# Performance work log

Measured on AMD Instinct MI355X. Metric: run time of the kernel, lower is better.

Reference implementation:

```python
import jax, jax.numpy as jnp
import numpy as np
from jax import lax

N, C, A, H, W = 32, 512, 256, 64, 64

def _maxpool2(t):
    # 2x2 max pool, stride 2, NCHW
    return lax.reduce_window(t, -jnp.inf, lax.max, (1, 1, 2, 2), (1, 1, 2, 2), 'VALID')

def setup_inputs() -> dict:
    key = jax.random.key(0)
    ks = jax.random.split(key, 5)
    return {
        'x': jax.random.normal(ks[0], (N, C, H, W), dtype=jnp.float32),
        'w_g': jax.random.normal(ks[1], (A, C), dtype=jnp.float32) * 0.02,
        'b_g': jax.random.normal(ks[2], (A,), dtype=jnp.float32) * 0.02,
        'w_phi': jax.random.normal(ks[3], (A, C), dtype=jnp.float32) * 0.02,
        'b_phi': jax.random.normal(ks[4], (A,), dtype=jnp.float32) * 0.02,
    }

def reference(x, w_g, b_g, w_phi, b_phi):
    n, c, h, w = x.shape
    # g: 1x1 conv in->attn, flattened spatial: (N, A, H*W)
    g_x = (jnp.einsum('nchw,ac->nahw', x, w_g) + b_g[None, :, None, None]).reshape(n, A, h * w)
    # theta: maxpool of x, (N, C, HW/4)
    theta_x = _maxpool2(x).reshape(n, c, -1)
    # phi: 1x1 conv then maxpool, (N, HW/4, A)
    phi_conv = jnp.einsum('nchw,ac->nahw', x, w_phi) + b_phi[None, :, None, None]
    phi_x = _maxpool2(phi_conv).reshape(n, A, -1)  # (N, A, HW/4)
    # channel-attention scores: (N, C, A)
    cmat = jnp.einsum('ncm,nam->nca', theta_x, phi_x)
    attn = jax.nn.softmax(cmat, axis=-1)
    # aggregate: (N, C, HW)
    y = jnp.einsum('nca,nal->ncl', attn, g_x)
    z = y.reshape(n, c, h, w)
    return z + x
```

## Files before the change

### kernel.cpp

```cpp
#include <hip/hip_runtime.h>


typedef _Float16 half8 __attribute__((ext_vector_type(8)));
typedef _Float16 half4v __attribute__((ext_vector_type(4)));
typedef float f32x4 __attribute__((ext_vector_type(4)));

#define NB 32
#define CD 512
#define AD 256
#define PD 4096
#define PPD 1024

#define OFF_XT    0UL
#define OFF_WC    134217728UL
#define OFF_THETA 134742016UL
#define OFF_GT    168296448UL
#define OFF_PHI   235405312UL
#define OFF_ATTN  252182528UL

#define GLOAD16(gp, lp) \
    __builtin_amdgcn_global_load_lds((const __attribute__((address_space(1))) void*)(gp), \
                                     (__attribute__((address_space(3))) void*)(lp), 16, 0, 0)

__device__ __forceinline__ int swz_off(int row, int q) {
    return row * 32 + ((q ^ ((row >> 1) & 3)) * 8);
}

template <int LD>
__device__ __forceinline__ void stage2(const _Float16* __restrict__ Ab,
                                       const _Float16* __restrict__ Bb,
                                       int k0, _Float16* bufA, _Float16* bufB, int t) {
#pragma unroll
    for (int j = 0; j < 4; ++j) {
        int idx = j * 256 + t;
        int ci = idx & 511;
        int row = ci >> 2, chP = ci & 3;
        int chL = chP ^ ((row >> 1) & 3);
        const _Float16* src = ((idx < 512) ? Ab : Bb) + (size_t)row * LD + k0 + chL * 8;
        _Float16* dst = ((idx < 512) ? bufA : bufB) + ci * 8;
        GLOAD16(src, dst);
    }
}

__global__ __launch_bounds__(256) void k_prep_w(const float* __restrict__ w_g,
                                                const float* __restrict__ w_phi,
                                                _Float16* __restrict__ Wc) {
    int idx4 = blockIdx.x * 256 + threadIdx.x;
    int flat = idx4 * 4;
    const float* src = (flat < AD * CD) ? (w_g + flat) : (w_phi + (flat - AD * CD));
    float4 v = *(const float4*)src;
    half4v h;
    h[0] = (_Float16)v.x; h[1] = (_Float16)v.y; h[2] = (_Float16)v.z; h[3] = (_Float16)v.w;
    *(half4v*)(Wc + flat) = h;
}

__global__ __launch_bounds__(256) void k_prep_x(const float* __restrict__ x,
                                                _Float16* __restrict__ xT,
                                                _Float16* __restrict__ theta) {
    __shared__ _Float16 tile[32 * 136];
    int pb = blockIdx.x;
    int cb = blockIdx.y;
    int n  = blockIdx.z;
    int t  = threadIdx.x;
    int p0 = pb * 128, c0 = cb * 32;

    const float* xbase = x + ((size_t)n * CD + c0) * PD + p0;
#pragma unroll
    for (int i = 0; i < 4; ++i) {
        int idx = i * 256 + t;
        int cl = idx >> 5;
        int ch = idx & 31;
        float4 v = *(const float4*)(xbase + (size_t)cl * PD + ch * 4);
        half4v h;
        h[0] = (_Float16)v.x; h[1] = (_Float16)v.y; h[2] = (_Float16)v.z; h[3] = (_Float16)v.w;
        *(half4v*)&tile[cl * 136 + ch * 4] = h;
    }
    __syncthreads();

    {
        int pl = t >> 1, ch = t & 1;
        _Float16 vals[16] __attribute__((aligned(16)));
#pragma unroll
        for (int j = 0; j < 16; ++j) vals[j] = tile[(ch * 16 + j) * 136 + pl];
        _Float16* dst = xT + ((size_t)n * PD + p0 + pl) * CD + c0 + ch * 16;
        *(uint4*)dst       = *(uint4*)&vals[0];
        *(uint4*)(dst + 8) = *(uint4*)&vals[8];
    }
    {
        int cl = t >> 3, u0 = (t & 7) * 4;
        _Float16 o[4] __attribute__((aligned(8)));
#pragma unroll
        for (int j = 0; j < 4; ++j) {
            int w2 = (u0 + j) * 2;
            float a0 = (float)tile[cl * 136 + w2];
            float a1 = (float)tile[cl * 136 + w2 + 1];
            float a2 = (float)tile[cl * 136 + 64 + w2];
            float a3 = (float)tile[cl * 136 + 64 + w2 + 1];
            o[j] = (_Float16)fmaxf(fmaxf(a0, a1), fmaxf(a2, a3));
        }
        _Float16* dst = theta + ((size_t)n * CD + c0 + cl) * PPD + pb * 32 + u0;
        *(uint2*)dst = *(uint2*)&o[0];
    }
}

__global__ __launch_bounds__(256) void k_gemm1(const _Float16* __restrict__ Wc,
                                               const _Float16* __restrict__ xT,
                                               const float* __restrict__ b_g,
                                               const float* __restrict__ b_phi,
                                               _Float16* __restrict__ gT,
                                               _Float16* __restrict__ phi) {
    __shared__ _Float16 smem[24576];

    int pb = blockIdx.x, ab = blockIdx.y, n = blockIdx.z;
    int a0 = ab * 128, p0 = pb * 128;
    int t = threadIdx.x;
    int w = t >> 6, l = t & 63;
    int ln = l & 15, q = l >> 4;
    int mw = (w >> 1) * 64, nw = (w & 1) * 64;

    const f32x4 vzero = {0.f, 0.f, 0.f, 0.f};
    f32x4 acc[4][4];
#pragma unroll
    for (int i = 0; i < 4; ++i)
#pragma unroll
        for (int j = 0; j < 4; ++j) acc[i][j] = vzero;

    const _Float16* Abase = Wc + (size_t)a0 * CD;
    const _Float16* Bbase = xT + ((size_t)n * PD + p0) * CD;

    stage2<CD>(Abase, Bbase, 0, smem, smem + 4096, t);
    stage2<CD>(Abase, Bbase, 32, smem + 8192, smem + 8192 + 4096, t);

#pragma unroll
    for (int ks = 0; ks < 15; ++ks) {
        asm volatile("s_waitcnt vmcnt(4)" ::: "memory");
        __builtin_amdgcn_s_barrier();
        __builtin_amdgcn_sched_barrier(0);
        if (ks + 2 < 16) {
            int ob = ((ks + 2) % 3) * 8192;
            stage2<CD>(Abase, Bbase, (ks + 2) * 32, smem + ob, smem + ob + 4096, t);
        }
        int oc = (ks % 3) * 8192;
        _Float16* As = smem + oc;
        _Float16* Bs = smem + oc + 4096;
        half8 af[4], bf[4];
#pragma unroll
        for (int mt = 0; mt < 4; ++mt) af[mt] = *(const half8*)&As[swz_off(mw + mt * 16 + ln, q)];
#pragma unroll
        for (int nt = 0; nt < 4; ++nt) bf[nt] = *(const half8*)&Bs[swz_off(nw + nt * 16 + ln, q)];
#pragma unroll
        for (int mt = 0; mt < 4; ++mt)
#pragma unroll
            for (int nt = 0; nt < 4; ++nt)
                acc[mt][nt] = __builtin_amdgcn_mfma_f32_16x16x32_f16(af[mt], bf[nt], acc[mt][nt], 0, 0, 0);
    }
    asm volatile("s_waitcnt vmcnt(0)" ::: "memory");
    __builtin_amdgcn_s_barrier();
    __builtin_amdgcn_sched_barrier(0);
    {
        int oc = (15 % 3) * 8192;
        _Float16* As = smem + oc;
        _Float16* Bs = smem + oc + 4096;
        half8 af[4], bf[4];
#pragma unroll
        for (int mt = 0; mt < 4; ++mt) af[mt] = *(const half8*)&As[swz_off(mw + mt * 16 + ln, q)];
#pragma unroll
        for (int nt = 0; nt < 4; ++nt) bf[nt] = *(const half8*)&Bs[swz_off(nw + nt * 16 + ln, q)];
#pragma unroll
        for (int mt = 0; mt < 4; ++mt)
#pragma unroll
            for (int nt = 0; nt < 4; ++nt)
                acc[mt][nt] = __builtin_amdgcn_mfma_f32_16x16x32_f16(af[mt], bf[nt], acc[mt][nt], 0, 0, 0);
    }
    __syncthreads();

    bool is_g = (a0 < 256);
    const float* bias = is_g ? b_g : b_phi;
    int abase = a0 - (is_g ? 0 : 256);
    float bv[4][4];
#pragma unroll
    for (int mt = 0; mt < 4; ++mt)
#pragma unroll
        for (int r = 0; r < 4; ++r) bv[mt][r] = bias[abase + mw + mt * 16 + q * 4 + r];

    _Float16* T = smem;
    if (is_g) {
#pragma unroll
        for (int mt = 0; mt < 4; ++mt)
#pragma unroll
            for (int nt = 0; nt < 4; ++nt)
#pragma unroll
                for (int r = 0; r < 4; ++r) {
                    int al = mw + mt * 16 + q * 4 + r;
                    int pl = nw + nt * 16 + ln;
                    T[pl * 136 + al] = (_Float16)(acc[mt][nt][r] + bv[mt][r]);
                }
        __syncthreads();
#pragma unroll
        for (int i = 0; i < 8; ++i) {
            int idx = i * 256 + t;
            int pl = idx >> 4, ch = idx & 15;
            uint4 v = *(uint4*)&T[pl * 136 + ch * 8];
            *(uint4*)(gT + ((size_t)n * PD + p0 + pl) * AD + a0 + ch * 8) = v;
        }
    } else {
#pragma unroll
        for (int mt = 0; mt < 4; ++mt)
#pragma unroll
            for (int nt = 0; nt < 4; ++nt)
#pragma unroll
                for (int r = 0; r < 4; ++r) {
                    int al = mw + mt * 16 + q * 4 + r;
                    int pl = nw + nt * 16 + ln;
                    T[al * 136 + pl] = (_Float16)(acc[mt][nt][r] + bv[mt][r]);
                }
        __syncthreads();
        int al = t >> 1, hf = t & 1;
        _Float16 o[16] __attribute__((aligned(16)));
#pragma unroll
        for (int j = 0; j < 16; ++j) {
            int u = hf * 16 + j;
            float v0 = (float)T[al * 136 + 2 * u];
            float v1 = (float)T[al * 136 + 2 * u + 1];
            float v2 = (float)T[al * 136 + 64 + 2 * u];
            float v3 = (float)T[al * 136 + 64 + 2 * u + 1];
            o[j] = (_Float16)fmaxf(fmaxf(v0, v1), fmaxf(v2, v3));
        }
        _Float16* dst = phi + ((size_t)n * AD + (a0 - 256) + al) * PPD + pb * 32 + hf * 16;
        *(uint4*)dst       = *(uint4*)&o[0];
        *(uint4*)(dst + 8) = *(uint4*)&o[8];
    }
}

__global__ __launch_bounds__(256) void k_gemm2(const _Float16* __restrict__ theta,
                                               const _Float16* __restrict__ phi,
                                               _Float16* __restrict__ attn) {
    __shared__ float red[3 * 64 * 65];
    int cb = blockIdx.x;
    int n  = blockIdx.y;
    int t = threadIdx.x, w = t >> 6, l = t & 63;
    int ln = l & 15, q = l >> 4;
    int c0 = cb * 16;

    const _Float16* Ab = theta + ((size_t)n * CD + c0 + ln) * PPD + w * 256;
    const _Float16* Bb = phi + ((size_t)n * AD + ln) * PPD + w * 256;

    const f32x4 vzero = {0.f, 0.f, 0.f, 0.f};
    f32x4 acc[16];
#pragma unroll
    for (int i = 0; i < 16; ++i) acc[i] = vzero;

    for (int k0 = 0; k0 < 256; k0 += 32) {
        half8 af = *(const half8*)(Ab + k0 + q * 8);
#pragma unroll
        for (int nt = 0; nt < 16; ++nt) {
            half8 bf = *(const half8*)(Bb + (size_t)nt * 16 * PPD + k0 + q * 8);
            acc[nt] = __builtin_amdgcn_mfma_f32_16x16x32_f16(af, bf, acc[nt], 0, 0, 0);
        }
    }

    if (w > 0) {
        float* dst = red + (w - 1) * 64 * 65 + l * 65;
#pragma unroll
        for (int nt = 0; nt < 16; ++nt)
#pragma unroll
            for (int r = 0; r < 4; ++r) dst[nt * 4 + r] = acc[nt][r];
    }
    __syncthreads();
    if (w == 0) {
#pragma unroll
        for (int j = 0; j < 3; ++j) {
            const float* src = red + j * 64 * 65 + l * 65;
#pragma unroll
            for (int nt = 0; nt < 16; ++nt)
#pragma unroll
                for (int r = 0; r < 4; ++r) acc[nt][r] += src[nt * 4 + r];
        }
#pragma unroll
        for (int r = 0; r < 4; ++r) {
            float m = -1e30f;
#pragma unroll
            for (int nt = 0; nt < 16; ++nt) m = fmaxf(m, acc[nt][r]);
#pragma unroll
            for (int s = 1; s < 16; s <<= 1) m = fmaxf(m, __shfl_xor(m, s, 64));
            float sum = 0.f;
#pragma unroll
            for (int nt = 0; nt < 16; ++nt) {
                float e = __expf(acc[nt][r] - m);
                acc[nt][r] = e;
                sum += e;
            }
#pragma unroll
            for (int s = 1; s < 16; s <<= 1) sum += __shfl_xor(sum, s, 64);
            float inv = 1.0f / sum;
            int c = c0 + q * 4 + r;
            _Float16* dst = attn + ((size_t)n * CD + c) * AD + ln;
#pragma unroll
            for (int nt = 0; nt < 16; ++nt) dst[nt * 16] = (_Float16)(acc[nt][r] * inv);
        }
    }
}

__global__ __launch_bounds__(256) void k_gemm3(const _Float16* __restrict__ attn,
                                               const _Float16* __restrict__ gT,
                                               const float* __restrict__ x,
                                               float* __restrict__ out) {
    __shared__ _Float16 smem[24576];

    int pb = blockIdx.x, cb = blockIdx.y, n = blockIdx.z;
    int c0 = cb * 128, p0 = pb * 128;
    int t = threadIdx.x;
    int w = t >> 6, l = t & 63;
    int ln = l & 15, q = l >> 4;
    int mw = (w >> 1) * 64, nw = (w & 1) * 64;

    const f32x4 vzero = {0.f, 0.f, 0.f, 0.f};
    f32x4 acc[4][4];
#pragma unroll
    for (int i = 0; i < 4; ++i)
#pragma unroll
        for (int j = 0; j < 4; ++j) acc[i][j] = vzero;

    const _Float16* Abase = attn + ((size_t)n * CD + c0) * AD;
    const _Float16* Bbase = gT + ((size_t)n * PD + p0) * AD;

    stage2<AD>(Abase, Bbase, 0, smem, smem + 4096, t);
    stage2<AD>(Abase, Bbase, 32, smem + 8192, smem + 8192 + 4096, t);

#pragma unroll
    for (int ks = 0; ks < 7; ++ks) {
        asm volatile("s_waitcnt vmcnt(4)" ::: "memory");
        __builtin_amdgcn_s_barrier();
        __builtin_amdgcn_sched_barrier(0);
        if (ks + 2 < 8) {
            int ob = ((ks + 2) % 3) * 8192;
            stage2<AD>(Abase, Bbase, (ks + 2) * 32, smem + ob, smem + ob + 4096, t);
        }
        int oc = (ks % 3) * 8192;
        _Float16* As = smem + oc;
        _Float16* Bs = smem + oc + 4096;
        half8 af[4], bf[4];
#pragma unroll
        for (int mt = 0; mt < 4; ++mt) af[mt] = *(const half8*)&Bs[swz_off(mw + mt * 16 + ln, q)];
#pragma unroll
        for (int nt = 0; nt < 4; ++nt) bf[nt] = *(const half8*)&As[swz_off(nw + nt * 16 + ln, q)];
#pragma unroll
        for (int mt = 0; mt < 4; ++mt)
#pragma unroll
            for (int nt = 0; nt < 4; ++nt)
                acc[mt][nt] = __builtin_amdgcn_mfma_f32_16x16x32_f16(af[mt], bf[nt], acc[mt][nt], 0, 0, 0);
    }
    asm volatile("s_waitcnt vmcnt(0)" ::: "memory");
    __builtin_amdgcn_s_barrier();
    __builtin_amdgcn_sched_barrier(0);
    {
        int oc = (7 % 3) * 8192;
        _Float16* As = smem + oc;
        _Float16* Bs = smem + oc + 4096;
        half8 af[4], bf[4];
#pragma unroll
        for (int mt = 0; mt < 4; ++mt) af[mt] = *(const half8*)&Bs[swz_off(mw + mt * 16 + ln, q)];
#pragma unroll
        for (int nt = 0; nt < 4; ++nt) bf[nt] = *(const half8*)&As[swz_off(nw + nt * 16 + ln, q)];
#pragma unroll
        for (int mt = 0; mt < 4; ++mt)
#pragma unroll
            for (int nt = 0; nt < 4; ++nt)
                acc[mt][nt] = __builtin_amdgcn_mfma_f32_16x16x32_f16(af[mt], bf[nt], acc[mt][nt], 0, 0, 0);
    }

#pragma unroll
    for (int mt = 0; mt < 4; ++mt) {
        int p = p0 + mw + mt * 16 + q * 4;
        size_t offs[4];
        f32x4 xv[4];
#pragma unroll
        for (int nt = 0; nt < 4; ++nt) {
            int c = c0 + nw + nt * 16 + ln;
            offs[nt] = ((size_t)n * CD + c) * PD + p;
            xv[nt] = __builtin_nontemporal_load((const f32x4*)(x + offs[nt]));
        }
#pragma unroll
        for (int nt = 0; nt < 4; ++nt) {
            f32x4 r = acc[mt][nt] + xv[nt];
            __builtin_nontemporal_store(r, (f32x4*)(out + offs[nt]));
        }
    }
}

extern "C" void kernel_launch(void* const* d_in, const int* in_sizes, int n_in,
                              void* d_out, int out_size, void* d_ws, size_t ws_size,
                              hipStream_t stream) {
    const float* x     = (const float*)d_in[0];
    const float* w_g   = (const float*)d_in[1];
    const float* b_g   = (const float*)d_in[2];
    const float* w_phi = (const float*)d_in[3];
    const float* b_phi = (const float*)d_in[4];
    float* out = (float*)d_out;

    char* ws = (char*)d_ws;
    _Float16* xT    = (_Float16*)(ws + OFF_XT);
    _Float16* Wc    = (_Float16*)(ws + OFF_WC);
    _Float16* theta = (_Float16*)(ws + OFF_THETA);
    _Float16* gT    = (_Float16*)(ws + OFF_GT);
    _Float16* phi   = (_Float16*)(ws + OFF_PHI);
    _Float16* attn  = (_Float16*)(ws + OFF_ATTN);

    k_prep_w<<<dim3(256), 256, 0, stream>>>(w_g, w_phi, Wc);
    k_prep_x<<<dim3(32, 16, 32), 256, 0, stream>>>(x, xT, theta);
    k_gemm1<<<dim3(32, 4, 32), 256, 0, stream>>>(Wc, xT, b_g, b_phi, gT, phi);
    k_gemm2<<<dim3(32, 32), 256, 0, stream>>>(theta, phi, attn);
    k_gemm3<<<dim3(32, 4, 32), 256, 0, stream>>>(attn, gT, x, out);
}
```

Before: 776.7 us.

## Load attn fragments directly to registers and double-buffer only gT in LDS

The final GEMM kernel no longer stages the attn tile through LDS. Each lane reads its attn fragments straight from global memory into registers, one k-step ahead. Only the gT tile is staged via global_load_lds, in a two-buffer ring instead of three, which cuts LDS from 48KB to 16KB and may raise occupancy. The epilogue now loads all 16 residual x vectors before any store, and those loads are regular rather than nontemporal. The risks are extra register pressure and uncoalesced direct global reads of attn rows. The vmcnt(4) wait count is also reused even though the number of outstanding loads has changed.

```diff
diff --git a/kernel.cpp b/kernel.cpp
--- a/kernel.cpp
+++ b/kernel.cpp
@@ -305,7 +305,7 @@
                                                const _Float16* __restrict__ gT,
                                                const float* __restrict__ x,
                                                float* __restrict__ out) {
-    __shared__ _Float16 smem[24576];
+    __shared__ _Float16 smem[8192];
 
     int pb = blockIdx.x, cb = blockIdx.y, n = blockIdx.z;
     int c0 = cb * 128, p0 = pb * 128;
@@ -321,71 +321,71 @@
 #pragma unroll
         for (int j = 0; j < 4; ++j) acc[i][j] = vzero;
 
-    const _Float16* Abase = attn + ((size_t)n * CD + c0) * AD;
     const _Float16* Bbase = gT + ((size_t)n * PD + p0) * AD;
-
-    stage2<AD>(Abase, Bbase, 0, smem, smem + 4096, t);
-    stage2<AD>(Abase, Bbase, 32, smem + 8192, smem + 8192 + 4096, t);
-
-#pragma unroll
-    for (int ks = 0; ks < 7; ++ks) {
+    const _Float16* brow[4];
+#pragma unroll
+    for (int nt = 0; nt < 4; ++nt)
+        brow[nt] = attn + ((size_t)n * CD + c0 + nw + nt * 16 + ln) * AD + q * 8;
+
+    auto stageB = [&](int k0, _Float16* buf) {
+#pragma unroll
+        for (int j = 0; j < 2; ++j) {
+            int idx = j * 256 + t;
+            int row = idx >> 2, chP = idx & 3;
+            int chL = chP ^ ((row >> 1) & 3);
+            GLOAD16(Bbase + (size_t)row * AD + k0 + chL * 8, buf + idx * 8);
+        }
+    };
+
+    half8 bfA[4], bfB[4];
+
+    stageB(0, smem);
+    __builtin_amdgcn_sched_barrier(0);
+#pragma unroll
+    for (int nt = 0; nt < 4; ++nt) bfA[nt] = *(const half8*)(brow[nt]);
+
+    auto step = [&](int ks, _Float16* Bs_cur, _Float16* Bs_nxt,
+                    half8 (&bfc)[4], half8 (&bfn)[4], bool issue) {
         asm volatile("s_waitcnt vmcnt(4)" ::: "memory");
         __builtin_amdgcn_s_barrier();
         __builtin_amdgcn_sched_barrier(0);
-        if (ks + 2 < 8) {
-            int ob = ((ks + 2) % 3) * 8192;
-            stage2<AD>(Abase, Bbase, (ks + 2) * 32, smem + ob, smem + ob + 4096, t);
-        }
-        int oc = (ks % 3) * 8192;
-        _Float16* As = smem + oc;
-        _Float16* Bs = smem + oc + 4096;
-        half8 af[4], bf[4];
-#pragma unroll
-        for (int mt = 0; mt < 4; ++mt) af[mt] = *(const half8*)&Bs[swz_off(mw + mt * 16 + ln, q)];
-#pragma unroll
-        for (int nt = 0; nt < 4; ++nt) bf[nt] = *(const half8*)&As[swz_off(nw + nt * 16 + ln, q)];
+        if (issue) {
+            stageB((ks + 1) * 32, Bs_nxt);
+            __builtin_amdgcn_sched_barrier(0);
+#pragma unroll
+            for (int nt = 0; nt < 4; ++nt) bfn[nt] = *(const half8*)(brow[nt] + (ks + 1) * 32);
+        }
+        half8 af[4];
+#pragma unroll
+        for (int mt = 0; mt < 4; ++mt) af[mt] = *(const half8*)&Bs_cur[swz_off(mw + mt * 16 + ln, q)];
 #pragma unroll
         for (int mt = 0; mt < 4; ++mt)
 #pragma unroll
             for (int nt = 0; nt < 4; ++nt)
-                acc[mt][nt] = __builtin_amdgcn_mfma_f32_16x16x32_f16(af[mt], bf[nt], acc[mt][nt], 0, 0, 0);
-    }
-    asm volatile("s_waitcnt vmcnt(0)" ::: "memory");
-    __builtin_amdgcn_s_barrier();
-    __builtin_amdgcn_sched_barrier(0);
-    {
-        int oc = (7 % 3) * 8192;
-        _Float16* As = smem + oc;
-        _Float16* Bs = smem + oc + 4096;
-        half8 af[4], bf[4];
-#pragma unroll
-        for (int mt = 0; mt < 4; ++mt) af[mt] = *(const half8*)&Bs[swz_off(mw + mt * 16 + ln, q)];
-#pragma unroll
-        for (int nt = 0; nt < 4; ++nt) bf[nt] = *(const half8*)&As[swz_off(nw + nt * 16 + ln, q)];
-#pragma unroll
-        for (int mt = 0; mt < 4; ++mt)
-#pragma unroll
-            for (int nt = 0; nt < 4; ++nt)
-                acc[mt][nt] = __builtin_amdgcn_mfma_f32_16x16x32_f16(af[mt], bf[nt], acc[mt][nt], 0, 0, 0);
-    }
-
-#pragma unroll
-    for (int mt = 0; mt < 4; ++mt) {
-        int p = p0 + mw + mt * 16 + q * 4;
-        size_t offs[4];
-        f32x4 xv[4];
+                acc[mt][nt] = __builtin_amdgcn_mfma_f32_16x16x32_f16(af[mt], bfc[nt], acc[mt][nt], 0, 0, 0);
+    };
+
+    _Float16* b0 = smem;
+    _Float16* b1 = smem + 4096;
+    for (int ks2 = 0; ks2 < 4; ++ks2) {
+        step(2 * ks2,     b0, b1, bfA, bfB, true);
+        step(2 * ks2 + 1, b1, b0, bfB, bfA, 2 * ks2 + 1 < 7);
+    }
+
+    size_t ebase = ((size_t)n * CD + c0 + nw + ln) * PD + (size_t)(p0 + mw + q * 4);
+    f32x4 xv[4][4];
+#pragma unroll
+    for (int mt = 0; mt < 4; ++mt)
+#pragma unroll
+        for (int nt = 0; nt < 4; ++nt)
+            xv[mt][nt] = *(const f32x4*)(x + ebase + (size_t)nt * 16 * PD + mt * 16);
+#pragma unroll
+    for (int mt = 0; mt < 4; ++mt)
 #pragma unroll
         for (int nt = 0; nt < 4; ++nt) {
-            int c = c0 + nw + nt * 16 + ln;
-            offs[nt] = ((size_t)n * CD + c) * PD + p;
-            xv[nt] = __builtin_nontemporal_load((const f32x4*)(x + offs[nt]));
-        }
-#pragma unroll
-        for (int nt = 0; nt < 4; ++nt) {
-            f32x4 r = acc[mt][nt] + xv[nt];
-            __builtin_nontemporal_store(r, (f32x4*)(out + offs[nt]));
-        }
-    }
+            f32x4 r = acc[mt][nt] + xv[mt][nt];
+            __builtin_nontemporal_store(r, (f32x4*)(out + ebase + (size_t)nt * 16 * PD + mt * 16));
+        }
 }
 
 extern "C" void kernel_launch(void* const* d_in, const int* in_sizes, int n_in,
```

Measured after the change: 762.5 us. Within noise of the previous version (-1.8%).
